# Kernel tuning notes

Hardware: AMD Instinct MI355X
Metric: run time of the kernel (lower is better)

The kernel has to match this reference:

```python
import jax, jax.numpy as jnp
import numpy as np

C = 256   # embedding_dim
B = 16
N = 2048
BN_EPS = 1e-5


def _sa_params(key, c):
    ks = jax.random.split(key, 8)
    s = 1.0 / np.sqrt(c)
    return dict(
        Wq=jax.random.normal(ks[0], (c // 2, c), jnp.float32) * s,
        Wk=jax.random.normal(ks[1], (c // 2, c), jnp.float32) * s,
        Wv=jax.random.normal(ks[2], (c, c), jnp.float32) * s,
        bv=jax.random.normal(ks[3], (c,), jnp.float32) * 0.01,
        Wt=jax.random.normal(ks[4], (c, c), jnp.float32) * s,
        bt=jax.random.normal(ks[5], (c,), jnp.float32) * 0.01,
        gamma=jnp.ones((c,), jnp.float32),
        beta=jnp.zeros((c,), jnp.float32),
    )


def setup_inputs() -> dict:
    key = jax.random.key(0)
    kx, k1, k2 = jax.random.split(key, 3)
    inp = {"x": jax.random.normal(kx, (B, C, N), jnp.float32)}
    for tag, kk in (("1", k1), ("2", k2)):
        for name, v in _sa_params(kk, C).items():
            inp[name + tag] = v
    return inp


def _sa_layer(x, Wq, Wk, Wv, bv, Wt, bt, gamma, beta):
    # 1x1 conv == per-point linear: [B,C,N]
    x_q = jnp.einsum('oc,bcn->bno', Wq, x)            # [B,N,C/2]
    x_k = jnp.einsum('oc,bcn->bon', Wk, x)            # [B,C/2,N]
    x_v = jnp.einsum('oc,bcn->bon', Wv, x) + bv[None, :, None]
    energy = jnp.einsum('bnc,bcm->bnm', x_q, x_k)     # [B,N,N]
    attn = jax.nn.softmax(energy, axis=-1)
    # offset-attention column-wise L1 renorm
    attn = attn / (1e-9 + attn.sum(axis=1, keepdims=True))
    x_r = jnp.einsum('bcn,bnm->bcm', x_v, attn)       # [B,C,N]
    h = x - x_r
    h = jnp.einsum('oc,bcn->bon', Wt, h) + bt[None, :, None]
    # BatchNorm1d (training mode, biased var over batch+points per channel)
    mean = h.mean(axis=(0, 2), keepdims=True)
    var = jnp.mean((h - mean) ** 2, axis=(0, 2), keepdims=True)
    h = (h - mean) * jax.lax.rsqrt(var + BN_EPS)
    h = h * gamma[None, :, None] + beta[None, :, None]
    return x + jax.nn.relu(h)


def reference(x,
              Wq1, Wk1, Wv1, bv1, Wt1, bt1, gamma1, beta1,
              Wq2, Wk2, Wv2, bv2, Wt2, bt2, gamma2, beta2):
    x1 = _sa_layer(x, Wq1, Wk1, Wv1, bv1, Wt1, bt1, gamma1, beta1)
    x2 = _sa_layer(x1, Wq2, Wk2, Wv2, bv2, Wt2, bt2, gamma2, beta2)
    return jnp.concatenate((x1, x2), axis=1)          # [B,2C,N]
```

## Files before the change

### kernel.cpp

```cpp
#include <hip/hip_runtime.h>

#define DI __device__ __forceinline__

typedef _Float16 f16_t;
typedef _Float16 f16x8 __attribute__((ext_vector_type(8)));
typedef float    f32x4 __attribute__((ext_vector_type(4)));

static_assert(sizeof(f16x8) == 16, "f16x8 must be 16B");

#define B_  16
#define C_  256
#define CH_ 128
#define N_  2048

DI f32x4 fzero(){ f32x4 z = {0.f,0.f,0.f,0.f}; return z; }
DI f16x8 ldg8(const f16_t* p){ return *(const f16x8*)p; }
DI f32x4 mfma16(f16x8 a, f16x8 b, f32x4 c){
  return __builtin_amdgcn_mfma_f32_16x16x32_f16(a, b, c, 0, 0, 0);
}
DI void split2(float v, f16_t& hi, f16_t& lo){
  hi = (f16_t)v; lo = (f16_t)(v - (float)hi);
}
DI int swz_b(int i){ return ((i&7)<<1) | ((i>>3)&1); }

#define GLL16(src, dst) __builtin_amdgcn_global_load_lds( \
    (const __attribute__((address_space(1))) void*)(src), \
    (__attribute__((address_space(3))) void*)(dst), 16, 0, 0)

__global__ void k_wconv(const float* q1,const float* k1,const float* v1,const float* t1,
                        const float* q2,const float* k2,const float* v2,const float* t2,
                        f16_t* out){
  int i = blockIdx.x*256 + threadIdx.x;
  int l = (i >= 196608) ? 1 : 0;
  int r = i - l*196608;
  const float* s; long dbase;
  if(r < 32768){ s = l? q2:q1; dbase = 0; }
  else if(r < 65536){ r -= 32768; s = l? k2:k1; dbase = 65536; }
  else if(r < 131072){ r -= 65536; s = l? v2:v1; dbase = 131072; }
  else { r -= 131072; s = l? t2:t1; dbase = 262144; }
  int o = r >> 8, c = r & 255;
  float v = s[o*256 + c];
  f16_t hi, lo; split2(v, hi, lo);
  f16_t* d = out + (long)l*393216 + dbase + (long)o*512;
  d[c] = hi; d[c+256] = lo;
}

__global__ void k_transpose(const float* __restrict__ X, long bstride,
                            f16_t* __restrict__ XtS){
  int b = blockIdx.x, n0 = blockIdx.y*32, c0 = blockIdx.z*64;
  __shared__ float tl[32][65];
  int t = threadIdx.x;
  int nn = t & 31, cr = t >> 5;
  const float* src = X + (long)b*bstride + n0 + nn;
  #pragma unroll
  for(int i=0;i<8;i++){
    int cc = cr + i*8;
    tl[nn][cc] = src[(long)(c0+cc)*N_];
  }
  __syncthreads();
  int n2 = t >> 3, cq = (t & 7)*8;
  __align__(16) f16_t hi8[8], lo8[8];
  #pragma unroll
  for(int j=0;j<8;j++) split2(tl[n2][cq+j], hi8[j], lo8[j]);
  f16_t* dst = XtS + ((long)b*N_ + n0 + n2)*512 + c0 + cq;
  *(f16x8*)dst         = *(f16x8*)hi8;
  *(f16x8*)(dst + 256) = *(f16x8*)lo8;
}

template<int LGX, int SPLIT_OUT, int BIAS, int DUAL>
__global__ __launch_bounds__(256) void k_gemm3(
    const f16_t* __restrict__ A, long sA,
    const f16_t* __restrict__ Bt, long sB,
    f16_t* __restrict__ out, int ldo, long sO,
    const float* __restrict__ bias, long dualoff)
{
  int i = blockIdx.x;
  int b = swz_b(i);
  int r = i>>4;
  int m0 = (r & ((1<<LGX)-1))*64, n0 = (r >> LGX)*64;
  int t = threadIdx.x, w = t>>6, l = t&63, lr = l&15, lg = l>>4;
  const f16_t* Ab = A + (long)b*sA + (long)(m0 + w*16 + lr)*512;
  const f16_t* Bb = Bt + (long)b*sB;
  f32x4 acc[4];
  #pragma unroll
  for(int i2=0;i2<4;i2++) acc[i2] = fzero();
  for(int k=0;k<256;k+=32){
    f16x8 ah = ldg8(Ab + k + lg*8);
    f16x8 al = ldg8(Ab + 256 + k + lg*8);
    #pragma unroll
    for(int ns=0;ns<4;ns++){
      const f16_t* brow = Bb + (long)(n0 + ns*16 + lr)*512;
      f16x8 bh = ldg8(brow + k + lg*8);
      f16x8 bl = ldg8(brow + 256 + k + lg*8);
      acc[ns] = mfma16(ah, bh, acc[ns]);
      acc[ns] = mfma16(ah, bl, acc[ns]);
      acc[ns] = mfma16(al, bh, acc[ns]);
    }
  }
  f16_t* ob = out + (long)b*sO;
  #pragma unroll
  for(int ns=0;ns<4;ns++){
    #pragma unroll
    for(int j=0;j<4;j++){
      int row = m0 + w*16 + lg*4 + j;
      int col = n0 + ns*16 + lr;
      float v = acc[ns][j];
      if(BIAS) v += bias[row];
      if(SPLIT_OUT){
        f16_t hi, lo; split2(v, hi, lo);
        f16_t* base = ob;
        if(DUAL && col >= 128) base = ob + (dualoff - 128);
        base[(long)row*ldo + col]       = hi;
        base[(long)row*ldo + col + 128] = lo;
      } else {
        ob[(long)row*ldo + col] = (f16_t)v;
      }
    }
  }
}

__global__ __launch_bounds__(256) void k_rowstats(
    const f16_t* __restrict__ xqS, const f16_t* __restrict__ xkS,
    float* __restrict__ rowoff)
{
  extern __shared__ __align__(16) char smem[];
  const int bi = blockIdx.x;
  const int b = swz_b(bi);
  const int n0 = (bi>>4)*64;
  const int t = threadIdx.x, w = t>>6, l = t&63, lr = l&15, lg = l>>4;

  const f16_t* qp = xqS + ((long)b*N_ + n0 + w*16 + lr)*256;
  f16x8 bqh[4], bql[4];
  #pragma unroll
  for(int k=0;k<4;k++){
    bqh[k] = ldg8(qp + k*32 + lg*8);
    bql[k] = ldg8(qp + 128 + k*32 + lg*8);
  }
  const f16_t* kb = xkS + (long)b*N_*256;

  const int krow_off = l>>5, kslot = l&31;
  const f16_t *ks0,*ks1,*ks2,*ks3;
  #define KINIT(r) { int row=(r*4+w)*2+krow_off; \
    ks##r = kb + (long)row*256 + ((kslot ^ (row&15))*8); }
  KINIT(0) KINIT(1) KINIT(2) KINIT(3)
  #undef KINIT
  #define KSTAGE(buf) do { char* kd = smem + (buf)*16384;                     \
    GLL16(ks0, kd + (0*4+w)*1024); GLL16(ks1, kd + (1*4+w)*1024);             \
    GLL16(ks2, kd + (2*4+w)*1024); GLL16(ks3, kd + (3*4+w)*1024); } while(0)
  #define KADV() do { ks0+=8192; ks1+=8192; ks2+=8192; ks3+=8192; } while(0)

  float rmax = -3e38f, rsum = 0.f;
  KSTAGE(0);

  #pragma unroll 1
  for(int i=0; i<64; i++){
    const int cur = i&1, nxt = cur^1;
    if(i<63){
      KADV();
      KSTAGE(nxt);
      asm volatile("s_waitcnt vmcnt(4)" ::: "memory");
    } else {
      asm volatile("s_waitcnt vmcnt(0)" ::: "memory");
    }
    asm volatile("s_barrier" ::: "memory");
    const char* kbuf = smem + cur*16384;
    #pragma unroll
    for(int s=0;s<2;s++){
      const char* krow = kbuf + (s*16 + lr)*512;
      f16x8 ah[4], al_[4];
      #pragma unroll
      for(int k=0;k<4;k++){
        ah[k]  = *(const f16x8*)(krow + ((((4*k+lg) ^ lr))<<4));
        al_[k] = *(const f16x8*)(krow + ((16 + (((4*k+lg)) ^ lr))<<4));
      }
      __builtin_amdgcn_s_setprio(1);
      f32x4 a1 = fzero(), a2 = fzero(), a3 = fzero();
      #pragma unroll
      for(int k=0;k<4;k++) a1 = mfma16(ah[k],  bqh[k], a1);
      #pragma unroll
      for(int k=0;k<4;k++) a2 = mfma16(ah[k],  bql[k], a2);
      #pragma unroll
      for(int k=0;k<4;k++) a3 = mfma16(al_[k], bqh[k], a3);
      __builtin_amdgcn_s_setprio(0);
      f32x4 acc = (a1 + a2) + a3;
      float vm = fmaxf(fmaxf(acc[0],acc[1]), fmaxf(acc[2],acc[3]));
      float nm = fmaxf(rmax, vm);
      rsum = rsum*__expf(rmax-nm)
           + __expf(acc[0]-nm)+__expf(acc[1]-nm)+__expf(acc[2]-nm)+__expf(acc[3]-nm);
      rmax = nm;
    }
    asm volatile("s_barrier" ::: "memory");
  }
  #undef KSTAGE
  #undef KADV

  #pragma unroll
  for(int off=16; off<64; off<<=1){
    float om = __shfl_xor(rmax, off, 64);
    float os = __shfl_xor(rsum, off, 64);
    float nm = fmaxf(rmax, om);
    rsum = rsum*__expf(rmax-nm) + os*__expf(om-nm);
    rmax = nm;
  }
  if(lg==0) rowoff[(long)b*N_ + n0 + w*16 + lr] = rmax + __logf(rsum);
}

__global__ __launch_bounds__(256) void k_apply(
    const f16_t* __restrict__ xqS, const f16_t* __restrict__ xkS,
    const f16_t* __restrict__ xv, const float* __restrict__ rowoff,
    const float* __restrict__ X, long xbstride, f16_t* __restrict__ h0T)
{
  extern __shared__ __align__(16) char smem[];
  const int bi = blockIdx.x;
  const int b = swz_b(bi);
  const int m0 = (bi>>4)*64;
  const int t = threadIdx.x, w = t>>6, l = t&63, lr = l&15, lg = l>>4;
  float* ro_s = (float*)(smem + 65536);
  {
    const float* rob = rowoff + (long)b*N_;
    *(f32x4*)(ro_s + t*4)        = *(const f32x4*)(rob + t*4);
    *(f32x4*)(ro_s + t*4 + 1024) = *(const f32x4*)(rob + t*4 + 1024);
  }

  const f16_t* akp = xkS + ((long)b*N_ + m0 + w*16 + lr)*256;
  f16x8 akh[4], akl[4];
  #pragma unroll
  for(int k=0;k<4;k++){
    akh[k] = ldg8(akp + k*32 + lg*8);
    akl[k] = ldg8(akp + 128 + k*32 + lg*8);
  }

  const f16_t* xqb = xqS + (long)b*N_*256;
  const f16_t* xvb = xv + (long)b*C_*N_;
  const int qperm = ((lr>>2)*8 + (lr&3));

  const int qrow_off = (l>>5), qslot = l&31;
  const int vc_off = (l>>2), vslot = l&3;

  const f16_t *qs0,*qs1,*qs2,*qs3,*vs0,*vs1,*vs2,*vs3;
  #define PINIT(r) { int qrow=(r*4+w)*2+qrow_off;                             \
    int qsw=(qrow&3)|(((qrow>>3)&3)<<2);                                      \
    qs##r = xqb + (long)qrow*256 + ((qslot ^ qsw)*8);                         \
    int vc=(r*4+w)*16+vc_off;                                                 \
    vs##r = xvb + (long)vc*N_ + ((vslot ^ (vc&3))*8); }
  PINIT(0) PINIT(1) PINIT(2) PINIT(3)
  #undef PINIT
  #define STAGE(buf) do {                                                     \
    char* qd = smem + (buf)*16384;                                            \
    char* vd = smem + 32768 + (buf)*16384;                                    \
    GLL16(qs0, qd + (0*4+w)*1024); GLL16(vs0, vd + (0*4+w)*1024);             \
    GLL16(qs1, qd + (1*4+w)*1024); GLL16(vs1, vd + (1*4+w)*1024);             \
    GLL16(qs2, qd + (2*4+w)*1024); GLL16(vs2, vd + (2*4+w)*1024);             \
    GLL16(qs3, qd + (3*4+w)*1024); GLL16(vs3, vd + (3*4+w)*1024); } while(0)
  #define PADV() do { qs0+=8192; qs1+=8192; qs2+=8192; qs3+=8192;             \
    vs0+=32; vs1+=32; vs2+=32; vs3+=32; } while(0)

  f32x4 y[16];
  #pragma unroll
  for(int i2=0;i2<16;i2++) y[i2] = fzero();
  float cs = 0.f, cm = -3e38f;

  __syncthreads();
  STAGE(0);

  const int vsl = (lg ^ (lr&3)) << 4;

  #pragma unroll 1
  for(int i=0; i<64; i++){
    const int cur = i&1, nxt = cur^1;
    const int n0 = i*32;
    if(i<63){
      PADV();
      STAGE(nxt);
      asm volatile("s_waitcnt vmcnt(8)" ::: "memory");
    } else {
      asm volatile("s_waitcnt vmcnt(0)" ::: "memory");
    }
    asm volatile("s_barrier" ::: "memory");
    const char* qb = smem + cur*16384;
    const char* vb = smem + 32768 + cur*16384;
    float g[2][4];
    #pragma unroll
    for(int s2=0;s2<2;s2++){
      const int rl = qperm + s2*4;
      const char* qrow = qb + rl*512;
      f16x8 qh[4], ql[4];
      #pragma unroll
      for(int k=0;k<4;k++){
        qh[k] = *(const f16x8*)(qrow + (((4*k + lg) ^ lr)<<4));
        ql[k] = *(const f16x8*)(qrow + 256 + (((4*k + lg) ^ lr)<<4));
      }
      __builtin_amdgcn_s_setprio(1);
      f32x4 e1 = fzero(), e2 = fzero(), e3 = fzero();
      #pragma unroll
      for(int k=0;k<4;k++) e1 = mfma16(qh[k], akh[k], e1);
      #pragma unroll
      for(int k=0;k<4;k++) e2 = mfma16(ql[k], akh[k], e2);
      #pragma unroll
      for(int k=0;k<4;k++) e3 = mfma16(qh[k], akl[k], e3);
      __builtin_amdgcn_s_setprio(0);
      f32x4 e = (e1 + e2) + e3;
      f32x4 ro4 = *(const f32x4*)(ro_s + n0 + lg*8 + s2*4);
      #pragma unroll
      for(int j=0;j<4;j++) g[s2][j] = e[j] - ro4[j];
    }
    float v = fmaxf(fmaxf(fmaxf(g[0][0],g[0][1]), fmaxf(g[0][2],g[0][3])),
                    fmaxf(fmaxf(g[1][0],g[1][1]), fmaxf(g[1][2],g[1][3])));
    v = fmaxf(v, __shfl_xor(v, 16, 64));
    v = fmaxf(v, __shfl_xor(v, 32, 64));
    bool need = v > cm + 8.f;
    float fj = need ? __expf(cm - v) : 1.f;
    if(need) cm = v;
    cs *= fj;
    __align__(16) f16_t pv[8];
    #pragma unroll
    for(int s2=0;s2<2;s2++){
      #pragma unroll
      for(int j=0;j<4;j++){
        float p = __expf(g[s2][j] - cm);
        f16_t pb = (f16_t)p;
        cs += (float)pb;
        pv[s2*4+j] = pb;
      }
    }
    f16x8 pfrag = *(const f16x8*)pv;
    if(__any(need)){
      #pragma unroll
      for(int cf=0;cf<16;cf++){
        #pragma unroll
        for(int j2=0;j2<4;j2++) y[cf][j2] *= fj;
      }
    }
    __builtin_amdgcn_s_setprio(1);
    #pragma unroll
    for(int cf=0;cf<16;cf++){
      f16x8 av = *(const f16x8*)(vb + (cf*16 + lr)*64 + vsl);
      y[cf] = mfma16(av, pfrag, y[cf]);
    }
    __builtin_amdgcn_s_setprio(0);
    asm volatile("s_barrier" ::: "memory");
  }
  #undef STAGE
  #undef PADV

  cs += __shfl_xor(cs, 16, 64);
  cs += __shfl_xor(cs, 32, 64);
  float inv = 1.f/(1e-9f*__expf(-cm) + cs);

  f16_t* H = (f16_t*)(smem + 49152);
  const int mq = t&63, cq = t>>6;
  const float* Xb = X + (long)b*xbstride + m0;
  uint4* dstb = (uint4*)(h0T + ((long)b*N_ + m0)*C_);
  #pragma unroll
  for(int half=0; half<2; half++){
    #pragma unroll
    for(int cf8=0; cf8<8; cf8++){
      int cf = half*8 + cf8;
      #pragma unroll
      for(int j=0;j<4;j++){
        int cl = cf8*16 + lg*4 + j;
        int m  = w*16 + lr;
        *(f16_t*)((char*)H + m*256 + ((((cl>>3) ^ (m&7))<<4) | ((cl&7)<<1)))
          = (f16_t)(y[cf][j]*inv);
      }
    }
    __syncthreads();
    #pragma unroll 4
    for(int ci=0; ci<32; ci++){
      int cl = cq*32 + ci;
      int c  = half*128 + cl;
      f16_t* hp = (f16_t*)((char*)H + mq*256 + ((((cl>>3) ^ (mq&7))<<4) | ((cl&7)<<1)));
      *hp = (f16_t)(Xb[(long)c*N_ + mq] - (float)*hp);
    }
    __syncthreads();
    {
      const uint4* src = (const uint4*)H;
      for(int i2=t;i2<1024;i2+=256){
        int row = i2>>4, slot = i2&15;
        dstb[row*32 + half*16 + slot] = src[(i2 & ~15) | (slot ^ (row&7))];
      }
    }
    __syncthreads();
  }
}

__global__ __launch_bounds__(256) void k_wt_bn(
    const f16_t* __restrict__ WtS, const f16_t* __restrict__ h0T,
    const float* __restrict__ bt,
    f16_t* __restrict__ h1, float* __restrict__ bnacc)
{
  int i = blockIdx.x;
  int b = swz_b(i);
  int r = i>>4;
  int o0 = (r&3)*64, m0 = (r>>2)*64;
  int t=threadIdx.x, w=t>>6, l=t&63, lr=l&15, lg=l>>4;
  const f16_t* Arow = WtS + (long)(o0 + w*16 + lr)*512;
  const f16_t* Bb = h0T + (long)b*N_*C_;
  f32x4 acc[4];
  #pragma unroll
  for(int i2=0;i2<4;i2++) acc[i2] = fzero();
  for(int k=0;k<C_;k+=32){
    f16x8 afh = ldg8(Arow + k + lg*8);
    f16x8 afl = ldg8(Arow + 256 + k + lg*8);
    #pragma unroll
    for(int ms=0;ms<4;ms++){
      f16x8 bf_ = ldg8(Bb + (long)(m0 + ms*16 + lr)*C_ + k + lg*8);
      acc[ms] = mfma16(afh, bf_, acc[ms]);
      acc[ms] = mfma16(afl, bf_, acc[ms]);
    }
  }
  float s1[4]={0.f,0.f,0.f,0.f}, s2v[4]={0.f,0.f,0.f,0.f};
  f16_t* h1b = h1 + (long)b*C_*N_;
  #pragma unroll
  for(int j=0;j<4;j++){
    int o = o0 + w*16 + lg*4 + j;
    float bias = bt[o];
    #pragma unroll
    for(int ms=0;ms<4;ms++){
      float v = acc[ms][j] + bias;
      h1b[(long)o*N_ + m0 + ms*16 + lr] = (f16_t)v;
      s1[j] += v; s2v[j] += v*v;
    }
  }
  #pragma unroll
  for(int off=1; off<16; off<<=1){
    #pragma unroll
    for(int j=0;j<4;j++){ s1[j]+=__shfl_xor(s1[j],off,64); s2v[j]+=__shfl_xor(s2v[j],off,64); }
  }
  if(lr==0){
    #pragma unroll
    for(int j=0;j<4;j++){
      int o = o0 + w*16 + lg*4 + j;
      atomicAdd(&bnacc[o], s1[j]);
      atomicAdd(&bnacc[256+o], s2v[j]);
    }
  }
}

__global__ void k_out(const f16_t* __restrict__ h1, const float* __restrict__ X, long xbstride,
                      const float* __restrict__ bnacc, const float* __restrict__ gamma,
                      const float* __restrict__ beta, float* __restrict__ out, long ocoff){
  long i = (long)blockIdx.x*256 + threadIdx.x;
  long e = i*8;
  int b = (int)(e >> 19);
  int rem = (int)(e & 524287);
  int c = rem >> 11;
  float mean = bnacc[c] * (1.f/32768.f);
  float var  = bnacc[256+c] * (1.f/32768.f) - mean*mean;
  float sc = gamma[c] * rsqrtf(var + 1e-5f);
  float sh = beta[c] - mean*sc;
  f16x8 hv = *(const f16x8*)(h1 + e);
  const float* xb = X + (long)b*xbstride + rem;
  float4 xr0 = *(const float4*)xb;
  float4 xr1 = *(const float4*)(xb + 4);
  float4 o0, o1;
  o0.x = xr0.x + fmaxf(fmaf((float)hv[0], sc, sh), 0.f);
  o0.y = xr0.y + fmaxf(fmaf((float)hv[1], sc, sh), 0.f);
  o0.z = xr0.z + fmaxf(fmaf((float)hv[2], sc, sh), 0.f);
  o0.w = xr0.w + fmaxf(fmaf((float)hv[3], sc, sh), 0.f);
  o1.x = xr1.x + fmaxf(fmaf((float)hv[4], sc, sh), 0.f);
  o1.y = xr1.y + fmaxf(fmaf((float)hv[5], sc, sh), 0.f);
  o1.z = xr1.z + fmaxf(fmaf((float)hv[6], sc, sh), 0.f);
  o1.w = xr1.w + fmaxf(fmaf((float)hv[7], sc, sh), 0.f);
  float* ob = out + (long)b*(512L*N_) + ocoff + rem;
  *(float4*)ob       = o0;
  *(float4*)(ob + 4) = o1;
}

extern "C" void kernel_launch(void* const* d_in, const int* in_sizes, int n_in,
                              void* d_out, int out_size, void* d_ws, size_t ws_size,
                              hipStream_t stream){
  (void)in_sizes; (void)n_in; (void)out_size; (void)ws_size;
  const float* x = (const float*)d_in[0];
  const float *Wf[2][4], *bv[2], *bt[2], *gm[2], *bb[2];
  for(int l=0;l<2;l++){
    int base = 1 + l*8;
    Wf[l][0]=(const float*)d_in[base+0];
    Wf[l][1]=(const float*)d_in[base+1];
    Wf[l][2]=(const float*)d_in[base+2];
    bv[l]   =(const float*)d_in[base+3];
    Wf[l][3]=(const float*)d_in[base+4];
    bt[l]   =(const float*)d_in[base+5];
    gm[l]   =(const float*)d_in[base+6];
    bb[l]   =(const float*)d_in[base+7];
  }
  char* ws = (char*)d_ws;
  size_t off = 0;
  auto alloc = [&](size_t bytes){ size_t o = off; off += (bytes + 255) & ~(size_t)255; return o; };
  size_t oXt = alloc((size_t)B_*N_*512*2);
  size_t oXq = alloc((size_t)B_*N_*256*2);
  size_t oXk = alloc((size_t)B_*N_*256*2);
  size_t oXv = alloc((size_t)B_*C_*N_*2);
  size_t oH0 = alloc((size_t)B_*N_*C_*2);
  size_t oRo = alloc((size_t)B_*N_*4);
  size_t oBn = alloc(2*512*4);
  size_t oW  = alloc((size_t)786432*2);

  hipMemsetAsync(ws + oBn, 0, 2*512*4, stream);
  k_wconv<<<1536,256,0,stream>>>(Wf[0][0],Wf[0][1],Wf[0][2],Wf[0][3],
                                 Wf[1][0],Wf[1][1],Wf[1][2],Wf[1][3],
                                 (f16_t*)(ws+oW));
  float* dout = (float*)d_out;
  f16_t* H1 = (f16_t*)(ws + oXq);
  const long XKOFF = ((long)(oXk - oXq)) / 2;
  for(int l=0;l<2;l++){
    const float* Xl = l ? dout : x;
    long xbs = l ? 512L*N_ : 256L*N_;
    const f16_t* WqS = (const f16_t*)(ws+oW) + (size_t)l*393216;
    const f16_t* WvS = WqS + 131072;
    const f16_t* WtS = WqS + 262144;
    f16_t* XtS = (f16_t*)(ws+oXt);
    f16_t* Xq  = (f16_t*)(ws+oXq);
    f16_t* Xk  = (f16_t*)(ws+oXk);
    f16_t* Xv  = (f16_t*)(ws+oXv);
    f16_t* H0  = (f16_t*)(ws+oH0);
    float* Ro  = (float*)(ws+oRo);
    float* Bn  = (float*)(ws+oBn) + l*512;

    k_transpose<<<dim3(B_, N_/32, C_/64),256,0,stream>>>(Xl, xbs, XtS);
    k_gemm3<5,1,0,1><<<2048,256,0,stream>>>(XtS, (long)N_*512, WqS, 0L,
                                            Xq, 256, (long)N_*256, nullptr, XKOFF);
    k_gemm3<2,0,1,0><<<2048,256,0,stream>>>(WvS, 0L, XtS, (long)N_*512,
                                            Xv, N_, (long)C_*N_, bv[l], 0L);
    k_rowstats<<<512,256,32768,stream>>>(Xq, Xk, Ro);
    k_apply<<<512,256,73728,stream>>>(Xq, Xk, Xv, Ro, Xl, xbs, H0);
    k_wt_bn<<<2048,256,0,stream>>>(WtS, H0, bt[l], H1, Bn);
    k_out<<<4096,256,0,stream>>>(H1, Xl, xbs, Bn, gm[l], bb[l], dout, (long)l*C_*N_);
  }
}
```

Baseline: 899.3 us.

## Widen rowstats blocks to 128 query rows and drop MFMA priority hints

k_rowstats now runs 512-thread blocks (8 waves) that each cover 128 query rows instead of 64. Each staged K tile is therefore reused by twice as many rows, which halves global K reads, and each thread issues two async loads per stage instead of four. The s_setprio bumps around the MFMA sections are removed from both the rowstats and apply kernels. k_apply now recomputes its staging addresses every iteration instead of keeping advancing pointers. On the last iteration it issues a dummy reload of the first tile so the vmcnt wait stays uniform, at the cost of some extra memory traffic and larger blocks with lower scheduling flexibility.

New measurement: 858.4 us. -4.5%, faster.

```diff
diff --git a/kernel.cpp b/kernel.cpp
--- a/kernel.cpp
+++ b/kernel.cpp
@@ -119,14 +119,14 @@
   }
 }
 
-__global__ __launch_bounds__(256) void k_rowstats(
+__global__ __launch_bounds__(512) void k_rowstats(
     const f16_t* __restrict__ xqS, const f16_t* __restrict__ xkS,
     float* __restrict__ rowoff)
 {
   extern __shared__ __align__(16) char smem[];
   const int bi = blockIdx.x;
   const int b = swz_b(bi);
-  const int n0 = (bi>>4)*64;
+  const int n0 = (bi>>4)*128;
   const int t = threadIdx.x, w = t>>6, l = t&63, lr = l&15, lg = l>>4;
 
   const f16_t* qp = xqS + ((long)b*N_ + n0 + w*16 + lr)*256;
@@ -139,15 +139,14 @@
   const f16_t* kb = xkS + (long)b*N_*256;
 
   const int krow_off = l>>5, kslot = l&31;
-  const f16_t *ks0,*ks1,*ks2,*ks3;
-  #define KINIT(r) { int row=(r*4+w)*2+krow_off; \
-    ks##r = kb + (long)row*256 + ((kslot ^ (row&15))*8); }
-  KINIT(0) KINIT(1) KINIT(2) KINIT(3)
-  #undef KINIT
+  const f16_t *ks0, *ks1;
+  { int row0 = w*2 + krow_off;
+    ks0 = kb + (long)row0*256 + ((kslot ^ (row0&15))*8);
+    int row1 = 16 + w*2 + krow_off;
+    ks1 = kb + (long)row1*256 + ((kslot ^ (row1&15))*8); }
+
   #define KSTAGE(buf) do { char* kd = smem + (buf)*16384;                     \
-    GLL16(ks0, kd + (0*4+w)*1024); GLL16(ks1, kd + (1*4+w)*1024);             \
-    GLL16(ks2, kd + (2*4+w)*1024); GLL16(ks3, kd + (3*4+w)*1024); } while(0)
-  #define KADV() do { ks0+=8192; ks1+=8192; ks2+=8192; ks3+=8192; } while(0)
+    GLL16(ks0, kd + w*1024); GLL16(ks1, kd + 8192 + w*1024); } while(0)
 
   float rmax = -3e38f, rsum = 0.f;
   KSTAGE(0);
@@ -156,9 +155,9 @@
   for(int i=0; i<64; i++){
     const int cur = i&1, nxt = cur^1;
     if(i<63){
-      KADV();
+      ks0 += 8192; ks1 += 8192;
       KSTAGE(nxt);
-      asm volatile("s_waitcnt vmcnt(4)" ::: "memory");
+      asm volatile("s_waitcnt vmcnt(2)" ::: "memory");
     } else {
       asm volatile("s_waitcnt vmcnt(0)" ::: "memory");
     }
@@ -173,7 +172,6 @@
         ah[k]  = *(const f16x8*)(krow + ((((4*k+lg) ^ lr))<<4));
         al_[k] = *(const f16x8*)(krow + ((16 + (((4*k+lg)) ^ lr))<<4));
       }
-      __builtin_amdgcn_s_setprio(1);
       f32x4 a1 = fzero(), a2 = fzero(), a3 = fzero();
       #pragma unroll
       for(int k=0;k<4;k++) a1 = mfma16(ah[k],  bqh[k], a1);
@@ -181,7 +179,6 @@
       for(int k=0;k<4;k++) a2 = mfma16(ah[k],  bql[k], a2);
       #pragma unroll
       for(int k=0;k<4;k++) a3 = mfma16(al_[k], bqh[k], a3);
-      __builtin_amdgcn_s_setprio(0);
       f32x4 acc = (a1 + a2) + a3;
       float vm = fmaxf(fmaxf(acc[0],acc[1]), fmaxf(acc[2],acc[3]));
       float nm = fmaxf(rmax, vm);
@@ -192,7 +189,6 @@
     asm volatile("s_barrier" ::: "memory");
   }
   #undef KSTAGE
-  #undef KADV
 
   #pragma unroll
   for(int off=16; off<64; off<<=1){
@@ -237,23 +233,20 @@
   const int qrow_off = (l>>5), qslot = l&31;
   const int vc_off = (l>>2), vslot = l&3;
 
-  const f16_t *qs0,*qs1,*qs2,*qs3,*vs0,*vs1,*vs2,*vs3;
-  #define PINIT(r) { int qrow=(r*4+w)*2+qrow_off;                             \
-    int qsw=(qrow&3)|(((qrow>>3)&3)<<2);                                      \
-    qs##r = xqb + (long)qrow*256 + ((qslot ^ qsw)*8);                         \
-    int vc=(r*4+w)*16+vc_off;                                                 \
-    vs##r = xvb + (long)vc*N_ + ((vslot ^ (vc&3))*8); }
-  PINIT(0) PINIT(1) PINIT(2) PINIT(3)
-  #undef PINIT
-  #define STAGE(buf) do {                                                     \
-    char* qd = smem + (buf)*16384;                                            \
-    char* vd = smem + 32768 + (buf)*16384;                                    \
-    GLL16(qs0, qd + (0*4+w)*1024); GLL16(vs0, vd + (0*4+w)*1024);             \
-    GLL16(qs1, qd + (1*4+w)*1024); GLL16(vs1, vd + (1*4+w)*1024);             \
-    GLL16(qs2, qd + (2*4+w)*1024); GLL16(vs2, vd + (2*4+w)*1024);             \
-    GLL16(qs3, qd + (3*4+w)*1024); GLL16(vs3, vd + (3*4+w)*1024); } while(0)
-  #define PADV() do { qs0+=8192; qs1+=8192; qs2+=8192; qs3+=8192;             \
-    vs0+=32; vs1+=32; vs2+=32; vs3+=32; } while(0)
+  #define STAGE(nn, nxtbuf) do {                                              \
+    char* qd = smem + (nxtbuf)*16384;                                         \
+    char* vd = smem + 32768 + (nxtbuf)*16384;                                 \
+    _Pragma("unroll")                                                         \
+    for(int r=0;r<4;r++){                                                     \
+      int qrow = (r*4+w)*2 + qrow_off;                                        \
+      int qsw  = (qrow&3) | (((qrow>>3)&3)<<2);                               \
+      const f16_t* qsrc = xqb + (long)((nn) + qrow)*256 + ((qslot ^ qsw)*8);  \
+      GLL16(qsrc, qd + (r*4+w)*1024);                                         \
+      int vc = (r*4+w)*16 + vc_off;                                           \
+      const f16_t* vsrc2 = xvb + (long)vc*N_ + (nn) + ((vslot ^ (vc&3))*8);   \
+      GLL16(vsrc2, vd + (r*4+w)*1024);                                        \
+    }                                                                         \
+  } while(0)
 
   f32x4 y[16];
   #pragma unroll
@@ -261,7 +254,7 @@
   float cs = 0.f, cm = -3e38f;
 
   __syncthreads();
-  STAGE(0);
+  STAGE(0, 0);
 
   const int vsl = (lg ^ (lr&3)) << 4;
 
@@ -269,13 +262,9 @@
   for(int i=0; i<64; i++){
     const int cur = i&1, nxt = cur^1;
     const int n0 = i*32;
-    if(i<63){
-      PADV();
-      STAGE(nxt);
-      asm volatile("s_waitcnt vmcnt(8)" ::: "memory");
-    } else {
-      asm volatile("s_waitcnt vmcnt(0)" ::: "memory");
-    }
+    const int nn = (i<63) ? (n0+32) : 0;
+    STAGE(nn, nxt);
+    asm volatile("s_waitcnt vmcnt(8)" ::: "memory");
     asm volatile("s_barrier" ::: "memory");
     const char* qb = smem + cur*16384;
     const char* vb = smem + 32768 + cur*16384;
@@ -290,7 +279,6 @@
         qh[k] = *(const f16x8*)(qrow + (((4*k + lg) ^ lr)<<4));
         ql[k] = *(const f16x8*)(qrow + 256 + (((4*k + lg) ^ lr)<<4));
       }
-      __builtin_amdgcn_s_setprio(1);
       f32x4 e1 = fzero(), e2 = fzero(), e3 = fzero();
       #pragma unroll
       for(int k=0;k<4;k++) e1 = mfma16(qh[k], akh[k], e1);
@@ -298,7 +286,6 @@
       for(int k=0;k<4;k++) e2 = mfma16(ql[k], akh[k], e2);
       #pragma unroll
       for(int k=0;k<4;k++) e3 = mfma16(qh[k], akl[k], e3);
-      __builtin_amdgcn_s_setprio(0);
       f32x4 e = (e1 + e2) + e3;
       f32x4 ro4 = *(const f32x4*)(ro_s + n0 + lg*8 + s2*4);
       #pragma unroll
@@ -331,17 +318,14 @@
         for(int j2=0;j2<4;j2++) y[cf][j2] *= fj;
       }
     }
-    __builtin_amdgcn_s_setprio(1);
     #pragma unroll
     for(int cf=0;cf<16;cf++){
       f16x8 av = *(const f16x8*)(vb + (cf*16 + lr)*64 + vsl);
       y[cf] = mfma16(av, pfrag, y[cf]);
     }
-    __builtin_amdgcn_s_setprio(0);
     asm volatile("s_barrier" ::: "memory");
   }
   #undef STAGE
-  #undef PADV
 
   cs += __shfl_xor(cs, 16, 64);
   cs += __shfl_xor(cs, 32, 64);
@@ -522,7 +506,7 @@
                                             Xq, 256, (long)N_*256, nullptr, XKOFF);
     k_gemm3<2,0,1,0><<<2048,256,0,stream>>>(WvS, 0L, XtS, (long)N_*512,
                                             Xv, N_, (long)C_*N_, bv[l], 0L);
-    k_rowstats<<<512,256,32768,stream>>>(Xq, Xk, Ro);
+    k_rowstats<<<256,512,32768,stream>>>(Xq, Xk, Ro);
     k_apply<<<512,256,73728,stream>>>(Xq, Xk, Xv, Ro, Xl, xbs, H0);
     k_wt_bn<<<2048,256,0,stream>>>(WtS, H0, bt[l], H1, Bn);
     k_out<<<4096,256,0,stream>>>(H1, Xl, xbs, Bn, gm[l], bb[l], dout, (long)l*C_*N_);
```

## Widen rowstats blocks, drop third split-precision MFMA on layer 2, trim apply rescale

Applied to the files above, without the earlier changes.

k_rowstats now runs 512-thread blocks covering 128 query rows, so each staged K tile is shared by twice as many waves, and each thread issues two K loads per stage instead of four. For the second layer the kernel is templated to skip the lo-K times hi-Q correction product, lowering the precision of the row log-sum-exp there. k_apply drops the s_setprio hints, checks for a max update with a wave-wide vote before the shuffles, and folds the accumulator rescale into that branch. Dropping the correction term only for layer 2 is a numerical shortcut that could move the rowstats normaliser away from the energies k_apply recomputes at full split precision.

New measurement: 856.8 us. 4.7% less time.

```diff
diff --git a/kernel.cpp b/kernel.cpp
--- a/kernel.cpp
+++ b/kernel.cpp
@@ -119,14 +119,15 @@
   }
 }
 
-__global__ __launch_bounds__(256) void k_rowstats(
+template<int T3>
+__global__ __launch_bounds__(512) void k_rowstats(
     const f16_t* __restrict__ xqS, const f16_t* __restrict__ xkS,
     float* __restrict__ rowoff)
 {
   extern __shared__ __align__(16) char smem[];
   const int bi = blockIdx.x;
   const int b = swz_b(bi);
-  const int n0 = (bi>>4)*64;
+  const int n0 = (bi>>4)*128;
   const int t = threadIdx.x, w = t>>6, l = t&63, lr = l&15, lg = l>>4;
 
   const f16_t* qp = xqS + ((long)b*N_ + n0 + w*16 + lr)*256;
@@ -139,15 +140,14 @@
   const f16_t* kb = xkS + (long)b*N_*256;
 
   const int krow_off = l>>5, kslot = l&31;
-  const f16_t *ks0,*ks1,*ks2,*ks3;
-  #define KINIT(r) { int row=(r*4+w)*2+krow_off; \
-    ks##r = kb + (long)row*256 + ((kslot ^ (row&15))*8); }
-  KINIT(0) KINIT(1) KINIT(2) KINIT(3)
-  #undef KINIT
+  const f16_t *ks0, *ks1;
+  { int row0 = w*2 + krow_off;
+    ks0 = kb + (long)row0*256 + ((kslot ^ (row0&15))*8);
+    int row1 = 16 + w*2 + krow_off;
+    ks1 = kb + (long)row1*256 + ((kslot ^ (row1&15))*8); }
+
   #define KSTAGE(buf) do { char* kd = smem + (buf)*16384;                     \
-    GLL16(ks0, kd + (0*4+w)*1024); GLL16(ks1, kd + (1*4+w)*1024);             \
-    GLL16(ks2, kd + (2*4+w)*1024); GLL16(ks3, kd + (3*4+w)*1024); } while(0)
-  #define KADV() do { ks0+=8192; ks1+=8192; ks2+=8192; ks3+=8192; } while(0)
+    GLL16(ks0, kd + w*1024); GLL16(ks1, kd + 8192 + w*1024); } while(0)
 
   float rmax = -3e38f, rsum = 0.f;
   KSTAGE(0);
@@ -156,9 +156,9 @@
   for(int i=0; i<64; i++){
     const int cur = i&1, nxt = cur^1;
     if(i<63){
-      KADV();
+      ks0 += 8192; ks1 += 8192;
       KSTAGE(nxt);
-      asm volatile("s_waitcnt vmcnt(4)" ::: "memory");
+      asm volatile("s_waitcnt vmcnt(2)" ::: "memory");
     } else {
       asm volatile("s_waitcnt vmcnt(0)" ::: "memory");
     }
@@ -167,21 +167,22 @@
     #pragma unroll
     for(int s=0;s<2;s++){
       const char* krow = kbuf + (s*16 + lr)*512;
-      f16x8 ah[4], al_[4];
-      #pragma unroll
-      for(int k=0;k<4;k++){
-        ah[k]  = *(const f16x8*)(krow + ((((4*k+lg) ^ lr))<<4));
-        al_[k] = *(const f16x8*)(krow + ((16 + (((4*k+lg)) ^ lr))<<4));
-      }
-      __builtin_amdgcn_s_setprio(1);
+      f16x8 ah[4];
+      #pragma unroll
+      for(int k=0;k<4;k++)
+        ah[k] = *(const f16x8*)(krow + ((((4*k+lg) ^ lr))<<4));
       f32x4 a1 = fzero(), a2 = fzero(), a3 = fzero();
       #pragma unroll
       for(int k=0;k<4;k++) a1 = mfma16(ah[k],  bqh[k], a1);
       #pragma unroll
       for(int k=0;k<4;k++) a2 = mfma16(ah[k],  bql[k], a2);
-      #pragma unroll
-      for(int k=0;k<4;k++) a3 = mfma16(al_[k], bqh[k], a3);
-      __builtin_amdgcn_s_setprio(0);
+      if(T3){
+        #pragma unroll
+        for(int k=0;k<4;k++){
+          f16x8 alk = *(const f16x8*)(krow + ((16 + (((4*k+lg)) ^ lr))<<4));
+          a3 = mfma16(alk, bqh[k], a3);
+        }
+      }
       f32x4 acc = (a1 + a2) + a3;
       float vm = fmaxf(fmaxf(acc[0],acc[1]), fmaxf(acc[2],acc[3]));
       float nm = fmaxf(rmax, vm);
@@ -192,7 +193,6 @@
     asm volatile("s_barrier" ::: "memory");
   }
   #undef KSTAGE
-  #undef KADV
 
   #pragma unroll
   for(int off=16; off<64; off<<=1){
@@ -290,7 +290,6 @@
         qh[k] = *(const f16x8*)(qrow + (((4*k + lg) ^ lr)<<4));
         ql[k] = *(const f16x8*)(qrow + 256 + (((4*k + lg) ^ lr)<<4));
       }
-      __builtin_amdgcn_s_setprio(1);
       f32x4 e1 = fzero(), e2 = fzero(), e3 = fzero();
       #pragma unroll
       for(int k=0;k<4;k++) e1 = mfma16(qh[k], akh[k], e1);
@@ -298,20 +297,29 @@
       for(int k=0;k<4;k++) e2 = mfma16(ql[k], akh[k], e2);
       #pragma unroll
       for(int k=0;k<4;k++) e3 = mfma16(qh[k], akl[k], e3);
-      __builtin_amdgcn_s_setprio(0);
       f32x4 e = (e1 + e2) + e3;
       f32x4 ro4 = *(const f32x4*)(ro_s + n0 + lg*8 + s2*4);
       #pragma unroll
       for(int j=0;j<4;j++) g[s2][j] = e[j] - ro4[j];
     }
-    float v = fmaxf(fmaxf(fmaxf(g[0][0],g[0][1]), fmaxf(g[0][2],g[0][3])),
-                    fmaxf(fmaxf(g[1][0],g[1][1]), fmaxf(g[1][2],g[1][3])));
-    v = fmaxf(v, __shfl_xor(v, 16, 64));
-    v = fmaxf(v, __shfl_xor(v, 32, 64));
-    bool need = v > cm + 8.f;
-    float fj = need ? __expf(cm - v) : 1.f;
-    if(need) cm = v;
-    cs *= fj;
+    float vl = fmaxf(fmaxf(fmaxf(g[0][0],g[0][1]), fmaxf(g[0][2],g[0][3])),
+                     fmaxf(fmaxf(g[1][0],g[1][1]), fmaxf(g[1][2],g[1][3])));
+    if(__any(vl > cm + 8.f)){
+      float v = vl;
+      v = fmaxf(v, __shfl_xor(v, 16, 64));
+      v = fmaxf(v, __shfl_xor(v, 32, 64));
+      bool need = v > cm + 8.f;
+      if(need){
+        float fj = __expf(cm - v);
+        cm = v;
+        cs *= fj;
+        #pragma unroll
+        for(int cf=0;cf<16;cf++){
+          #pragma unroll
+          for(int j2=0;j2<4;j2++) y[cf][j2] *= fj;
+        }
+      }
+    }
     __align__(16) f16_t pv[8];
     #pragma unroll
     for(int s2=0;s2<2;s2++){
@@ -324,20 +332,11 @@
       }
     }
     f16x8 pfrag = *(const f16x8*)pv;
-    if(__any(need)){
-      #pragma unroll
-      for(int cf=0;cf<16;cf++){
-        #pragma unroll
-        for(int j2=0;j2<4;j2++) y[cf][j2] *= fj;
-      }
-    }
-    __builtin_amdgcn_s_setprio(1);
     #pragma unroll
     for(int cf=0;cf<16;cf++){
       f16x8 av = *(const f16x8*)(vb + (cf*16 + lr)*64 + vsl);
       y[cf] = mfma16(av, pfrag, y[cf]);
     }
-    __builtin_amdgcn_s_setprio(0);
     asm volatile("s_barrier" ::: "memory");
   }
   #undef STAGE
@@ -522,7 +521,8 @@
                                             Xq, 256, (long)N_*256, nullptr, XKOFF);
     k_gemm3<2,0,1,0><<<2048,256,0,stream>>>(WvS, 0L, XtS, (long)N_*512,
                                             Xv, N_, (long)C_*N_, bv[l], 0L);
-    k_rowstats<<<512,256,32768,stream>>>(Xq, Xk, Ro);
+    if(l==0) k_rowstats<1><<<256,512,32768,stream>>>(Xq, Xk, Ro);
+    else     k_rowstats<0><<<256,512,32768,stream>>>(Xq, Xk, Ro);
     k_apply<<<512,256,73728,stream>>>(Xq, Xk, Xv, Ro, Xl, xbs, H0);
     k_wt_bn<<<2048,256,0,stream>>>(WtS, H0, bt[l], H1, Bn);
     k_out<<<4096,256,0,stream>>>(H1, Xl, xbs, Bn, gm[l], bb[l], dout, (long)l*C_*N_);
```
